# Kernel optimization log

Hardware: AMD Instinct MI355X
Metric: run time of the kernel (lower is better)

The kernel has to match this reference:

```python
import jax, jax.numpy as jnp
import numpy as np

B, N, C = 8, 4096, 512
NUM_HEADS = 8
HEAD_DIM = C // NUM_HEADS
POS_RES = 32  # only table with res <= max_resolution=32


def _interp_linear(pos, out_len):
    # F.interpolate(mode='linear', align_corners=False) along the length axis (axis 1)
    in_len = pos.shape[1]
    scale = in_len / out_len
    coords = (jnp.arange(out_len, dtype=jnp.float32) + 0.5) * scale - 0.5
    coords = jnp.clip(coords, 0.0, in_len - 1)
    i0 = jnp.floor(coords).astype(jnp.int32)
    i1 = jnp.minimum(i0 + 1, in_len - 1)
    w = (coords - i0.astype(jnp.float32))[None, :, None]
    return pos[:, i0, :] * (1.0 - w) + pos[:, i1, :] * w


def setup_inputs():
    key = jax.random.key(0)
    k = jax.random.split(key, 4)
    x = jax.random.normal(k[0], (B, N, C), jnp.float32)
    pos_32 = jax.random.normal(k[1], (1, POS_RES ** 3, C), jnp.float32)  # torch.randn init
    s = 1.0 / np.sqrt(C)
    w_qkv = jax.random.normal(k[2], (C, 3 * C), jnp.float32) * s
    b_qkv = jnp.zeros((3 * C,), jnp.float32)
    w_proj = jax.random.normal(k[3], (C, C), jnp.float32) * s
    b_proj = jnp.zeros((C,), jnp.float32)
    return {"x": x, "pos_32": pos_32, "w_qkv": w_qkv, "b_qkv": b_qkv,
            "w_proj": w_proj, "b_proj": b_proj, "resolution": 16}


def reference(x, pos_32, w_qkv, b_qkv, w_proj, b_proj, resolution):
    Bx, Nx, Cx = x.shape
    target_len = resolution ** 3  # 4096 -> nearest table pos_32 is interpolated down
    pos = pos_32 if pos_32.shape[1] == target_len else _interp_linear(pos_32, target_len)
    if pos.shape[1] == Nx:
        x = x + pos
    qkv = (x @ w_qkv + b_qkv).reshape(Bx, Nx, 3, NUM_HEADS, HEAD_DIM)
    q, k, v = qkv[:, :, 0], qkv[:, :, 1], qkv[:, :, 2]  # each [B, N, H, D]
    # Faithful to source: q,k,v are NOT permuted to [B,H,N,D], so q @ k.T
    # contracts head_dim per token, yielding [B, N, H, H] head-axis attention.
    attn = jnp.einsum('bnid,bnjd->bnij', q, k) / np.sqrt(HEAD_DIM)
    attn = jax.nn.softmax(attn, axis=-1)
    out = jnp.einsum('bnij,bnjd->bnid', attn, v)  # [B, N, H, D]
    # torch: .transpose(1, 2).reshape(B, N, C) -> flatten of [B, H, N, D]
    out = jnp.transpose(out, (0, 2, 1, 3)).reshape(Bx, Nx, Cx)
    return out @ w_proj + b_proj
```

## Files before the change

kernel.cpp:

```cpp
#include <hip/hip_runtime.h>
#include <hip/hip_bf16.h>

using bf16 = __hip_bfloat16;
typedef __attribute__((ext_vector_type(8))) short short8;
typedef __attribute__((ext_vector_type(4))) float f32x4;

#define AS1U(p) ((const __attribute__((address_space(1))) unsigned int*)(p))
#define AS3U(p) ((__attribute__((address_space(3))) unsigned int*)(p))

__device__ __forceinline__ float bflo(unsigned u) { return __uint_as_float(u << 16); }
__device__ __forceinline__ float bfhi(unsigned u) { return __uint_as_float(u & 0xffff0000u); }
__device__ __forceinline__ unsigned short f2bf(float f) {
    union { float f; unsigned u; } v{f};
    unsigned r = v.u + 0x7fffu + ((v.u >> 16) & 1u);
    return (unsigned short)(r >> 16);
}

__global__ __launch_bounds__(256) void kprep(const float* __restrict__ wq,
                                             const float* __restrict__ wp,
                                             const float* __restrict__ x,
                                             const float* __restrict__ pos,
                                             bf16* __restrict__ wqT,
                                             bf16* __restrict__ wpT,
                                             bf16* __restrict__ xp) {
    int bid = blockIdx.x;
    __shared__ float t[32][33];
    if (bid < 1024) {
        const float* in; bf16* out; int Cc, bx, by;
        if (bid < 768) { in = wq; out = wqT; Cc = 1536; bx = bid % 48; by = bid / 48; }
        else { int i = bid - 768; in = wp; out = wpT; Cc = 512; bx = i & 15; by = i >> 4; }
        const int R = 512;
        int tx = threadIdx.x & 31, ty = threadIdx.x >> 5;
        int c0 = bx * 32, r0 = by * 32;
#pragma unroll
        for (int i = 0; i < 4; ++i)
            t[ty + i * 8][tx] = in[(size_t)(r0 + ty + i * 8) * Cc + c0 + tx];
        __syncthreads();
#pragma unroll
        for (int i = 0; i < 4; ++i)
            out[(size_t)(c0 + ty + i * 8) * R + r0 + tx] = __float2bfloat16(t[tx][ty + i * 8]);
    } else {
        size_t idx4 = (size_t)(bid - 1024) * 256 + threadIdx.x;
        size_t e = idx4 * 4;
        int c = (int)(e & 511);
        size_t m = e >> 9;
        int n = (int)(m & 4095);
        float4 xv = *(const float4*)(x + e);
        float4 p3 = *(const float4*)(pos + (size_t)(n * 8 + 3) * 512 + c);
        float4 p4 = *(const float4*)(pos + (size_t)(n * 8 + 4) * 512 + c);
        unsigned r[2];
        float v0 = xv.x + 0.5f * (p3.x + p4.x);
        float v1 = xv.y + 0.5f * (p3.y + p4.y);
        float v2 = xv.z + 0.5f * (p3.z + p4.z);
        float v3 = xv.w + 0.5f * (p3.w + p4.w);
        r[0] = (unsigned)f2bf(v0) | ((unsigned)f2bf(v1) << 16);
        r[1] = (unsigned)f2bf(v2) | ((unsigned)f2bf(v3) << 16);
        *(uint2*)(xp + e) = *(uint2*)r;
    }
}


__global__ __launch_bounds__(512, 2) void kgemmP(const bf16* __restrict__ A,
                                                 const bf16* __restrict__ Bt,
                                                 const float* __restrict__ bias,
                                                 bf16* __restrict__ C) {
    constexpr int K = 512, N = 1536;
    __shared__ __align__(16) char smem[131072];
    const int tid = threadIdx.x;
    const int lane = tid & 63, wave = tid >> 6;
    const int wm = wave >> 2, wn = wave & 3;
    const int fr = lane & 15;
    const int g = lane >> 4;

    const int p_rd = (((fr & 1) << 2) | g) ^ ((fr >> 1) & 7);
    const int tbA = (wm * 64 + (fr >> 1)) * 128 + p_rd * 16;
    const int tbB = (wn * 32 + (fr >> 1)) * 128 + p_rd * 16;

    const int bid = blockIdx.x;
    const int bm = (bid & 127) << 8;
    const int bngrp = bid >> 7;

    const int q = (lane & 7) ^ (lane >> 3);
    const int srow = wave * 32 + 2 * (lane >> 3) + ((q >> 2) & 1);
    const int scol = (q & 3) * 8;
    const bf16* sA0 = A + (size_t)(bm + srow) * K + scol;
    const bf16* sA1 = A + (size_t)(bm + srow + 16) * K + scol;
    const bf16* b00 = Bt + (size_t)(bngrp * 768 +   0 + srow) * K + scol;
    const bf16* b01 = Bt + (size_t)(bngrp * 768 +  16 + srow) * K + scol;
    const bf16* b10 = b00 + (size_t)256 * K;
    const bf16* b11 = b01 + (size_t)256 * K;
    const bf16* b20 = b00 + (size_t)512 * K;
    const bf16* b21 = b01 + (size_t)512 * K;
    const int dA0 = wave * 2048, dA1 = wave * 2048 + 1024;

    auto stageA = [&](int kt, int slot) {
        char* d = smem + slot * 32768;
        __builtin_amdgcn_global_load_lds(AS1U(sA0 + kt * 32), AS3U(d + dA0), 16, 0, 0);
        __builtin_amdgcn_global_load_lds(AS1U(sA1 + kt * 32), AS3U(d + dA1), 16, 0, 0);
    };
    auto stageBp = [&](const bf16* p0, const bf16* p1, int kt, int slot) {
        char* d = smem + slot * 32768 + 16384;
        __builtin_amdgcn_global_load_lds(AS1U(p0 + kt * 32), AS3U(d + dA0), 16, 0, 0);
        __builtin_amdgcn_global_load_lds(AS1U(p1 + kt * 32), AS3U(d + dA1), 16, 0, 0);
    };

    f32x4 acc[8][4];

    stageA(0, 0); stageBp(b00, b01, 0, 0);
    stageA(1, 1); stageBp(b00, b01, 1, 1);
    stageA(2, 2); stageBp(b00, b01, 2, 2);
    asm volatile("s_waitcnt vmcnt(8)" ::: "memory");
    __builtin_amdgcn_s_barrier();

    const bf16 *curB0 = b00, *curB1 = b01, *nxtB0 = b10, *nxtB1 = b11;
    for (int j = 0; j < 3; ++j) {
#pragma unroll
        for (int i = 0; i < 8; ++i)
#pragma unroll
            for (int jj = 0; jj < 4; ++jj) acc[i][jj] = f32x4{0.f, 0.f, 0.f, 0.f};
#pragma unroll
        for (int t = 0; t < 16; ++t) {
            const int rd = t & 3, wrs = (t + 3) & 3;
            const char* pa = smem + rd * 32768;
            const char* pb = pa + 16384;
            if (t <= 12) { stageA(t + 3, wrs); stageBp(curB0, curB1, t + 3, wrs); }
            else if (j < 2) { stageA(t - 13, wrs); stageBp(nxtB0, nxtB1, t - 13, wrs); }
            short8 af[8], bfr[4];
#pragma unroll
            for (int mi = 0; mi < 8; ++mi) af[mi] = *(const short8*)(pa + tbA + mi * 1024);
#pragma unroll
            for (int nj = 0; nj < 4; ++nj) bfr[nj] = *(const short8*)(pb + tbB + nj * 1024);
#pragma unroll
            for (int mi = 0; mi < 8; ++mi)
#pragma unroll
                for (int nj = 0; nj < 4; ++nj)
                    acc[mi][nj] = __builtin_amdgcn_mfma_f32_16x16x32_bf16(af[mi], bfr[nj], acc[mi][nj], 0, 0, 0);
            asm volatile("s_waitcnt lgkmcnt(0)" ::: "memory");
            if (j < 2 || t <= 12)  asm volatile("s_waitcnt vmcnt(8)" ::: "memory");
            else if (t == 13)      asm volatile("s_waitcnt vmcnt(4)" ::: "memory");
            else if (t == 14)      asm volatile("s_waitcnt vmcnt(0)" ::: "memory");
            __builtin_amdgcn_sched_barrier(0);
            __builtin_amdgcn_s_barrier();
        }
        const int bn = bngrp * 768 + j * 256;
#pragma unroll
        for (int mi = 0; mi < 8; ++mi) {
#pragma unroll
            for (int nj = 0; nj < 4; ++nj) {
                int col = bn + wn * 64 + nj * 16 + fr;
                int row0 = bm + wm * 128 + mi * 16 + (lane >> 4) * 4;
                float bv = bias[col];
#pragma unroll
                for (int rr = 0; rr < 4; ++rr)
                    C[(size_t)(row0 + rr) * N + col] = (bf16)__float2bfloat16(acc[mi][nj][rr] + bv);
            }
        }
        curB0 = nxtB0; curB1 = nxtB1; nxtB0 = b20; nxtB1 = b21;
    }
}

template <typename OutT>
__global__ __launch_bounds__(512, 2) void kgemm8(const bf16* __restrict__ A,
                                                 const bf16* __restrict__ Bt,
                                                 const float* __restrict__ bias,
                                                 OutT* __restrict__ C,
                                                 int M, int N, int K_) {
    constexpr int K = 512;
    __shared__ __align__(16) char smem[131072];
    const int tid = threadIdx.x;
    const int lane = tid & 63, wave = tid >> 6;
    const int wm = wave >> 2, wn = wave & 3;
    const int fr = lane & 15;
    const int g = lane >> 4;

    const int p_rd = (((fr & 1) << 2) | g) ^ ((fr >> 1) & 7);
    const int tbA = (wm * 64 + (fr >> 1)) * 128 + p_rd * 16;
    const int tbB = (wn * 32 + (fr >> 1)) * 128 + p_rd * 16;

    const int ntn = N >> 8;
    const int nwg = gridDim.x;
    const int bid = blockIdx.x;
    const int swz = (bid & 7) * (nwg >> 3) + (bid >> 3);
    const int bm = (swz / ntn) << 8;
    const int bn = (swz % ntn) << 8;

    const int q = (lane & 7) ^ (lane >> 3);
    const int srow = wave * 32 + 2 * (lane >> 3) + ((q >> 2) & 1);
    const int scol = (q & 3) * 8;
    const bf16* sA[2]; const bf16* sB[2];
#pragma unroll
    for (int g2 = 0; g2 < 2; ++g2) {
        sA[g2] = A  + (size_t)(bm + srow + g2 * 16) * K + scol;
        sB[g2] = Bt + (size_t)(bn + srow + g2 * 16) * K + scol;
    }
    const int dA0 = wave * 2048, dA1 = wave * 2048 + 1024;

    f32x4 acc[8][4];
#pragma unroll
    for (int i = 0; i < 8; ++i)
#pragma unroll
        for (int j = 0; j < 4; ++j) acc[i][j] = f32x4{0.f, 0.f, 0.f, 0.f};

    auto stageA = [&](int kt, int slot) {
        char* d = smem + slot * 32768;
        __builtin_amdgcn_global_load_lds(AS1U(sA[0] + kt * 32), AS3U(d + dA0), 16, 0, 0);
        __builtin_amdgcn_global_load_lds(AS1U(sA[1] + kt * 32), AS3U(d + dA1), 16, 0, 0);
    };
    auto stageB = [&](int kt, int slot) {
        char* d = smem + slot * 32768 + 16384;
        __builtin_amdgcn_global_load_lds(AS1U(sB[0] + kt * 32), AS3U(d + dA0), 16, 0, 0);
        __builtin_amdgcn_global_load_lds(AS1U(sB[1] + kt * 32), AS3U(d + dA1), 16, 0, 0);
    };

    stageA(0, 0); stageB(0, 0);
    stageA(1, 1); stageB(1, 1);
    stageA(2, 2); stageB(2, 2);
    asm volatile("s_waitcnt vmcnt(8)" ::: "memory");
    __builtin_amdgcn_s_barrier();

#pragma unroll
    for (int t = 0; t < 16; ++t) {
        const int rd = t & 3, wrs = (t + 3) & 3;
        const char* pa = smem + rd * 32768;
        const char* pb = pa + 16384;
        if (t < 13) { stageA(t + 3, wrs); stageB(t + 3, wrs); }
        short8 af[8], bfr[4];
#pragma unroll
        for (int mi = 0; mi < 8; ++mi) af[mi] = *(const short8*)(pa + tbA + mi * 1024);
#pragma unroll
        for (int nj = 0; nj < 4; ++nj) bfr[nj] = *(const short8*)(pb + tbB + nj * 1024);
#pragma unroll
        for (int mi = 0; mi < 8; ++mi)
#pragma unroll
            for (int nj = 0; nj < 4; ++nj)
                acc[mi][nj] = __builtin_amdgcn_mfma_f32_16x16x32_bf16(af[mi], bfr[nj], acc[mi][nj], 0, 0, 0);
        asm volatile("s_waitcnt lgkmcnt(0)" ::: "memory");
        if (t <= 12)      asm volatile("s_waitcnt vmcnt(8)" ::: "memory");
        else if (t == 13) asm volatile("s_waitcnt vmcnt(4)" ::: "memory");
        else if (t == 14) asm volatile("s_waitcnt vmcnt(0)" ::: "memory");
        __builtin_amdgcn_sched_barrier(0);
        __builtin_amdgcn_s_barrier();
    }

#pragma unroll
    for (int mi = 0; mi < 8; ++mi) {
#pragma unroll
        for (int nj = 0; nj < 4; ++nj) {
            int col = bn + wn * 64 + nj * 16 + fr;
            int row0 = bm + wm * 128 + mi * 16 + (lane >> 4) * 4;
            float bv = bias[col];
#pragma unroll
            for (int rr = 0; rr < 4; ++rr) {
                float val = acc[mi][nj][rr] + bv;
                if constexpr (sizeof(OutT) == 2)
                    C[(size_t)(row0 + rr) * N + col] = (OutT)__float2bfloat16(val);
                else
                    C[(size_t)(row0 + rr) * N + col] = (OutT)val;
            }
        }
    }
}

__global__ __launch_bounds__(256) void kattn(const bf16* __restrict__ qkv,
                                             bf16* __restrict__ oscr) {
    int T = blockIdx.x * 256 + threadIdx.x;
    int token = T >> 3, head = T & 7;
    int b = token >> 12, n = token & 4095;
    const bf16* row = qkv + (size_t)token * 1536;

    uint4 qp[8];
#pragma unroll
    for (int c = 0; c < 8; ++c) qp[c] = *(const uint4*)(row + head * 64 + c * 8);

    float s[8];
#pragma unroll
    for (int j = 0; j < 8; ++j) {
        float acc = 0.f;
#pragma unroll
        for (int c = 0; c < 8; ++c) {
            uint4 kp = *(const uint4*)(row + 512 + j * 64 + c * 8);
            const unsigned* ku = &kp.x; const unsigned* qu = &qp[c].x;
#pragma unroll
            for (int w = 0; w < 4; ++w) {
                acc = fmaf(bflo(qu[w]), bflo(ku[w]), acc);
                acc = fmaf(bfhi(qu[w]), bfhi(ku[w]), acc);
            }
        }
        s[j] = acc * 0.125f;
    }
    float mx = s[0];
#pragma unroll
    for (int j = 1; j < 8; ++j) mx = fmaxf(mx, s[j]);
    float sum = 0.f;
#pragma unroll
    for (int j = 0; j < 8; ++j) { s[j] = __expf(s[j] - mx); sum += s[j]; }
    float inv = 1.f / sum;
#pragma unroll
    for (int j = 0; j < 8; ++j) s[j] *= inv;

    float o[64];
#pragma unroll
    for (int d = 0; d < 64; ++d) o[d] = 0.f;
#pragma unroll
    for (int j = 0; j < 8; ++j) {
        float pj = s[j];
#pragma unroll
        for (int c = 0; c < 8; ++c) {
            uint4 vp = *(const uint4*)(row + 1024 + j * 64 + c * 8);
            const unsigned* vu = &vp.x;
#pragma unroll
            for (int w = 0; w < 4; ++w) {
                o[c * 8 + w * 2]     = fmaf(pj, bflo(vu[w]), o[c * 8 + w * 2]);
                o[c * 8 + w * 2 + 1] = fmaf(pj, bfhi(vu[w]), o[c * 8 + w * 2 + 1]);
            }
        }
    }
    size_t orow = (size_t)b * 4096 + head * 512 + (n >> 3);
    bf16* op = oscr + orow * 512 + (n & 7) * 64;
#pragma unroll
    for (int c = 0; c < 8; ++c) {
        unsigned rr[4];
#pragma unroll
        for (int w = 0; w < 4; ++w)
            rr[w] = (unsigned)f2bf(o[c * 8 + w * 2]) | ((unsigned)f2bf(o[c * 8 + w * 2 + 1]) << 16);
        *(uint4*)(op + c * 8) = *(uint4*)rr;
    }
}

extern "C" void kernel_launch(void* const* d_in, const int* in_sizes, int n_in,
                              void* d_out, int out_size, void* d_ws, size_t ws_size,
                              hipStream_t stream) {
    const float* x      = (const float*)d_in[0];
    const float* pos32  = (const float*)d_in[1];
    const float* w_qkv  = (const float*)d_in[2];
    const float* b_qkv  = (const float*)d_in[3];
    const float* w_proj = (const float*)d_in[4];
    const float* b_proj = (const float*)d_in[5];

    char* ws = (char*)d_ws;
    bf16* xp   = (bf16*)(ws);
    bf16* qkv  = (bf16*)(ws + 33554432);
    bf16* wqT  = (bf16*)(ws + 134217728);
    bf16* wpT  = (bf16*)(ws + 135790592);
    bf16* ascr = xp;

    kprep<<<17408, 256, 0, stream>>>(w_qkv, w_proj, x, pos32, wqT, wpT, xp);
    kgemmP<<<256, 512, 0, stream>>>(xp, wqT, b_qkv, qkv);
    kattn<<<1024, 256, 0, stream>>>(qkv, ascr);
    kgemm8<float><<<256, 512, 0, stream>>>(ascr, wpT, b_proj, (float*)d_out, 32768, 512, 512);
}
```

Baseline: 159.9 us.

## Replace persistent 3-tile QKV GEMM with one-tile-per-block double-buffered GEMM

Result: faster. 144.6 us (-9.6%).

```diff
diff --git a/kernel.cpp b/kernel.cpp
--- a/kernel.cpp
+++ b/kernel.cpp
@@ -40,32 +40,37 @@
         for (int i = 0; i < 4; ++i)
             out[(size_t)(c0 + ty + i * 8) * R + r0 + tx] = __float2bfloat16(t[tx][ty + i * 8]);
     } else {
-        size_t idx4 = (size_t)(bid - 1024) * 256 + threadIdx.x;
-        size_t e = idx4 * 4;
+        size_t idx8 = (size_t)(bid - 1024) * 256 + threadIdx.x;
+        size_t e = idx8 * 8;
         int c = (int)(e & 511);
-        size_t m = e >> 9;
-        int n = (int)(m & 4095);
-        float4 xv = *(const float4*)(x + e);
-        float4 p3 = *(const float4*)(pos + (size_t)(n * 8 + 3) * 512 + c);
-        float4 p4 = *(const float4*)(pos + (size_t)(n * 8 + 4) * 512 + c);
-        unsigned r[2];
-        float v0 = xv.x + 0.5f * (p3.x + p4.x);
-        float v1 = xv.y + 0.5f * (p3.y + p4.y);
-        float v2 = xv.z + 0.5f * (p3.z + p4.z);
-        float v3 = xv.w + 0.5f * (p3.w + p4.w);
-        r[0] = (unsigned)f2bf(v0) | ((unsigned)f2bf(v1) << 16);
-        r[1] = (unsigned)f2bf(v2) | ((unsigned)f2bf(v3) << 16);
-        *(uint2*)(xp + e) = *(uint2*)r;
-    }
-}
-
-
-__global__ __launch_bounds__(512, 2) void kgemmP(const bf16* __restrict__ A,
+        int n = (int)((e >> 9) & 4095);
+        const float* xs = x + e;
+        const float* p3 = pos + (size_t)(n * 8 + 3) * 512 + c;
+        const float* p4 = pos + (size_t)(n * 8 + 4) * 512 + c;
+        unsigned r[4];
+#pragma unroll
+        for (int h = 0; h < 2; ++h) {
+            float4 xv = *(const float4*)(xs + h * 4);
+            float4 a = *(const float4*)(p3 + h * 4);
+            float4 b = *(const float4*)(p4 + h * 4);
+            float v0 = xv.x + 0.5f * (a.x + b.x);
+            float v1 = xv.y + 0.5f * (a.y + b.y);
+            float v2 = xv.z + 0.5f * (a.z + b.z);
+            float v3 = xv.w + 0.5f * (a.w + b.w);
+            r[h * 2]     = (unsigned)f2bf(v0) | ((unsigned)f2bf(v1) << 16);
+            r[h * 2 + 1] = (unsigned)f2bf(v2) | ((unsigned)f2bf(v3) << 16);
+        }
+        *(uint4*)(xp + e) = *(uint4*)r;
+    }
+}
+
+
+__global__ __launch_bounds__(512, 2) void kgemm2(const bf16* __restrict__ A,
                                                  const bf16* __restrict__ Bt,
                                                  const float* __restrict__ bias,
                                                  bf16* __restrict__ C) {
     constexpr int K = 512, N = 1536;
-    __shared__ __align__(16) char smem[131072];
+    __shared__ __align__(16) char smem[65536];
     const int tid = threadIdx.x;
     const int lane = tid & 63, wave = tid >> 6;
     const int wm = wave >> 2, wn = wave & 3;
@@ -76,86 +81,74 @@
     const int tbA = (wm * 64 + (fr >> 1)) * 128 + p_rd * 16;
     const int tbB = (wn * 32 + (fr >> 1)) * 128 + p_rd * 16;
 
+    const int ntn = N >> 8;
+    const int nwg = gridDim.x;
     const int bid = blockIdx.x;
-    const int bm = (bid & 127) << 8;
-    const int bngrp = bid >> 7;
+    const int swz = (bid & 7) * (nwg >> 3) + (bid >> 3);
+    const int bm = (swz / ntn) << 8;
+    const int bn = (swz % ntn) << 8;
 
     const int q = (lane & 7) ^ (lane >> 3);
     const int srow = wave * 32 + 2 * (lane >> 3) + ((q >> 2) & 1);
     const int scol = (q & 3) * 8;
-    const bf16* sA0 = A + (size_t)(bm + srow) * K + scol;
-    const bf16* sA1 = A + (size_t)(bm + srow + 16) * K + scol;
-    const bf16* b00 = Bt + (size_t)(bngrp * 768 +   0 + srow) * K + scol;
-    const bf16* b01 = Bt + (size_t)(bngrp * 768 +  16 + srow) * K + scol;
-    const bf16* b10 = b00 + (size_t)256 * K;
-    const bf16* b11 = b01 + (size_t)256 * K;
-    const bf16* b20 = b00 + (size_t)512 * K;
-    const bf16* b21 = b01 + (size_t)512 * K;
+    const bf16* sA[2]; const bf16* sB[2];
+#pragma unroll
+    for (int g2 = 0; g2 < 2; ++g2) {
+        sA[g2] = A  + (size_t)(bm + srow + g2 * 16) * K + scol;
+        sB[g2] = Bt + (size_t)(bn + srow + g2 * 16) * K + scol;
+    }
     const int dA0 = wave * 2048, dA1 = wave * 2048 + 1024;
 
-    auto stageA = [&](int kt, int slot) {
+    f32x4 acc[8][4];
+#pragma unroll
+    for (int i = 0; i < 8; ++i)
+#pragma unroll
+        for (int j = 0; j < 4; ++j) acc[i][j] = f32x4{0.f, 0.f, 0.f, 0.f};
+
+    auto stage = [&](int kt, int slot) {
         char* d = smem + slot * 32768;
-        __builtin_amdgcn_global_load_lds(AS1U(sA0 + kt * 32), AS3U(d + dA0), 16, 0, 0);
-        __builtin_amdgcn_global_load_lds(AS1U(sA1 + kt * 32), AS3U(d + dA1), 16, 0, 0);
+        __builtin_amdgcn_global_load_lds(AS1U(sA[0] + kt * 32), AS3U(d + dA0), 16, 0, 0);
+        __builtin_amdgcn_global_load_lds(AS1U(sA[1] + kt * 32), AS3U(d + dA1), 16, 0, 0);
+        __builtin_amdgcn_global_load_lds(AS1U(sB[0] + kt * 32), AS3U(d + 16384 + dA0), 16, 0, 0);
+        __builtin_amdgcn_global_load_lds(AS1U(sB[1] + kt * 32), AS3U(d + 16384 + dA1), 16, 0, 0);
     };
-    auto stageBp = [&](const bf16* p0, const bf16* p1, int kt, int slot) {
-        char* d = smem + slot * 32768 + 16384;
-        __builtin_amdgcn_global_load_lds(AS1U(p0 + kt * 32), AS3U(d + dA0), 16, 0, 0);
-        __builtin_amdgcn_global_load_lds(AS1U(p1 + kt * 32), AS3U(d + dA1), 16, 0, 0);
-    };
-
-    f32x4 acc[8][4];
-
-    stageA(0, 0); stageBp(b00, b01, 0, 0);
-    stageA(1, 1); stageBp(b00, b01, 1, 1);
-    stageA(2, 2); stageBp(b00, b01, 2, 2);
-    asm volatile("s_waitcnt vmcnt(8)" ::: "memory");
+
+    stage(0, 0);
+    asm volatile("s_waitcnt vmcnt(0)" ::: "memory");
     __builtin_amdgcn_s_barrier();
 
-    const bf16 *curB0 = b00, *curB1 = b01, *nxtB0 = b10, *nxtB1 = b11;
-    for (int j = 0; j < 3; ++j) {
-#pragma unroll
-        for (int i = 0; i < 8; ++i)
-#pragma unroll
-            for (int jj = 0; jj < 4; ++jj) acc[i][jj] = f32x4{0.f, 0.f, 0.f, 0.f};
-#pragma unroll
-        for (int t = 0; t < 16; ++t) {
-            const int rd = t & 3, wrs = (t + 3) & 3;
-            const char* pa = smem + rd * 32768;
-            const char* pb = pa + 16384;
-            if (t <= 12) { stageA(t + 3, wrs); stageBp(curB0, curB1, t + 3, wrs); }
-            else if (j < 2) { stageA(t - 13, wrs); stageBp(nxtB0, nxtB1, t - 13, wrs); }
-            short8 af[8], bfr[4];
-#pragma unroll
-            for (int mi = 0; mi < 8; ++mi) af[mi] = *(const short8*)(pa + tbA + mi * 1024);
-#pragma unroll
-            for (int nj = 0; nj < 4; ++nj) bfr[nj] = *(const short8*)(pb + tbB + nj * 1024);
-#pragma unroll
-            for (int mi = 0; mi < 8; ++mi)
-#pragma unroll
-                for (int nj = 0; nj < 4; ++nj)
-                    acc[mi][nj] = __builtin_amdgcn_mfma_f32_16x16x32_bf16(af[mi], bfr[nj], acc[mi][nj], 0, 0, 0);
-            asm volatile("s_waitcnt lgkmcnt(0)" ::: "memory");
-            if (j < 2 || t <= 12)  asm volatile("s_waitcnt vmcnt(8)" ::: "memory");
-            else if (t == 13)      asm volatile("s_waitcnt vmcnt(4)" ::: "memory");
-            else if (t == 14)      asm volatile("s_waitcnt vmcnt(0)" ::: "memory");
-            __builtin_amdgcn_sched_barrier(0);
-            __builtin_amdgcn_s_barrier();
-        }
-        const int bn = bngrp * 768 + j * 256;
-#pragma unroll
-        for (int mi = 0; mi < 8; ++mi) {
-#pragma unroll
-            for (int nj = 0; nj < 4; ++nj) {
-                int col = bn + wn * 64 + nj * 16 + fr;
-                int row0 = bm + wm * 128 + mi * 16 + (lane >> 4) * 4;
-                float bv = bias[col];
-#pragma unroll
-                for (int rr = 0; rr < 4; ++rr)
-                    C[(size_t)(row0 + rr) * N + col] = (bf16)__float2bfloat16(acc[mi][nj][rr] + bv);
-            }
-        }
-        curB0 = nxtB0; curB1 = nxtB1; nxtB0 = b20; nxtB1 = b21;
+#pragma unroll
+    for (int t = 0; t < 16; ++t) {
+        const char* pa = smem + (t & 1) * 32768;
+        const char* pb = pa + 16384;
+        if (t < 15) stage(t + 1, (t + 1) & 1);
+        short8 af[8], bfr[4];
+#pragma unroll
+        for (int mi = 0; mi < 8; ++mi) af[mi] = *(const short8*)(pa + tbA + mi * 1024);
+#pragma unroll
+        for (int nj = 0; nj < 4; ++nj) bfr[nj] = *(const short8*)(pb + tbB + nj * 1024);
+#pragma unroll
+        for (int mi = 0; mi < 8; ++mi)
+#pragma unroll
+            for (int nj = 0; nj < 4; ++nj)
+                acc[mi][nj] = __builtin_amdgcn_mfma_f32_16x16x32_bf16(af[mi], bfr[nj], acc[mi][nj], 0, 0, 0);
+        asm volatile("s_waitcnt lgkmcnt(0)" ::: "memory");
+        if (t < 15) asm volatile("s_waitcnt vmcnt(0)" ::: "memory");
+        __builtin_amdgcn_sched_barrier(0);
+        __builtin_amdgcn_s_barrier();
+    }
+
+#pragma unroll
+    for (int mi = 0; mi < 8; ++mi) {
+#pragma unroll
+        for (int nj = 0; nj < 4; ++nj) {
+            int col = bn + wn * 64 + nj * 16 + fr;
+            int row0 = bm + wm * 128 + mi * 16 + (lane >> 4) * 4;
+            float bv = bias[col];
+#pragma unroll
+            for (int rr = 0; rr < 4; ++rr)
+                C[(size_t)(row0 + rr) * N + col] = (bf16)__float2bfloat16(acc[mi][nj][rr] + bv);
+        }
     }
 }
 
@@ -344,8 +337,8 @@
     bf16* wpT  = (bf16*)(ws + 135790592);
     bf16* ascr = xp;
 
-    kprep<<<17408, 256, 0, stream>>>(w_qkv, w_proj, x, pos32, wqT, wpT, xp);
-    kgemmP<<<256, 512, 0, stream>>>(xp, wqT, b_qkv, qkv);
+    kprep<<<9216, 256, 0, stream>>>(w_qkv, w_proj, x, pos32, wqT, wpT, xp);
+    kgemm2<<<768, 512, 0, stream>>>(xp, wqT, b_qkv, qkv);
     kattn<<<1024, 256, 0, stream>>>(qkv, ascr);
     kgemm8<float><<<256, 512, 0, stream>>>(ascr, wpT, b_proj, (float*)d_out, 32768, 512, 512);
 }
```
